# Kernel optimization log

Measured on AMD Instinct MI355X. Metric: run time of the kernel, lower is better.

The kernel has to match this reference:

```python
import jax, jax.numpy as jnp
import numpy as np

B, PD, CD = 8192, 1024, 1024


def setup_inputs() -> dict:
    key = jax.random.key(0)
    ks = jax.random.split(key, 10)
    u = lambda k, shape: jax.random.uniform(k, shape, dtype=jnp.float32, minval=-0.05, maxval=0.05)
    return {
        "P": jax.random.normal(ks[0], (B, PD), dtype=jnp.float32),
        "C1": jax.random.normal(ks[1], (B, CD), dtype=jnp.float32),
        "C2": jax.random.normal(ks[2], (B, CD), dtype=jnp.float32),
        "C3": jax.random.normal(ks[3], (B, CD), dtype=jnp.float32),
        "C4": jax.random.normal(ks[4], (B, CD), dtype=jnp.float32),
        "GateWeight_P": u(ks[5], (PD, CD)),
        "GateWeight_C": u(ks[6], (CD, CD)),
        "GateBias": u(ks[7], (CD,)),
        "OutWeight": u(ks[8], (PD, CD)),
        "OutBias": u(ks[9], (CD, 1)),
    }


def reference(P, C1, C2, C3, C4, GateWeight_P, GateWeight_C, GateBias, OutWeight, OutBias):
    # Stack the 4 choice branches: [4, B, C]
    Cs = jnp.stack([C1, C2, C3, C4], axis=0)
    WP = P @ GateWeight_P                                  # [B, C]
    WC = jnp.einsum("kbc,cd->kbd", Cs, GateWeight_C)       # [4, B, C]
    g = jax.nn.sigmoid(WP[None] + WC + GateBias)           # [4, B, C]
    C_dash = Cs * g                                        # [4, B, C]
    WP_out = P @ OutWeight                                 # [B, C]
    scores = jnp.einsum("kbc,bc->kb", C_dash, WP_out)      # batch_dot axes=[1,1]
    bias = jnp.einsum("kbc,c->kb", C_dash, OutBias[:, 0])  # K.dot(C_dash, OutBias)
    return (scores + bias).T                               # [B, 4]
```

## Files before the change

kernel.cpp:

```cpp
#include <hip/hip_runtime.h>
#include <hip/hip_bf16.h>


#define B_  8192
#define PD_ 1024
#define CD_ 1024

typedef unsigned short ushort_t;
typedef unsigned int   uint_t;
typedef __attribute__((ext_vector_type(8))) short    short8;
typedef __attribute__((ext_vector_type(4))) float    floatx4;

__device__ __forceinline__ float bf2f(unsigned short u) {
    return __uint_as_float(((unsigned)u) << 16);
}
__device__ __forceinline__ unsigned short f2bf(float f) {
    unsigned u = __float_as_uint(f);
    unsigned r = u + 0x7FFFu + ((u >> 16) & 1u);
    return (unsigned short)(r >> 16);
}

__global__ __launch_bounds__(256) void prep_kernel(const float* __restrict__ P,
                                                   const float* __restrict__ C1,
                                                   const float* __restrict__ C2,
                                                   const float* __restrict__ C3,
                                                   const float* __restrict__ C4,
                                                   const float* __restrict__ GWP,
                                                   const float* __restrict__ OW,
                                                   const float* __restrict__ GWC,
                                                   ushort_t* __restrict__ Pb,
                                                   ushort_t* __restrict__ Call,
                                                   ushort_t* __restrict__ Wcat,
                                                   ushort_t* __restrict__ GWCt,
                                                   float* __restrict__ out) {
    const int bid = blockIdx.x;
    const int tid = threadIdx.x;
    if (bid < 40960) {
        const int seg = bid >> 13;
        const int i   = (bid & 8191) * 256 + tid;
        const float* src;
        ushort_t* dst;
        switch (seg) {
            case 0: src = P;  dst = Pb; break;
            case 1: src = C1; dst = Call; break;
            case 2: src = C2; dst = Call + (size_t)1 * B_ * CD_; break;
            case 3: src = C3; dst = Call + (size_t)2 * B_ * CD_; break;
            default: src = C4; dst = Call + (size_t)3 * B_ * CD_; break;
        }
        float4 v = ((const float4*)src)[i];
        ushort4 o;
        o.x = f2bf(v.x); o.y = f2bf(v.y); o.z = f2bf(v.z); o.w = f2bf(v.w);
        ((ushort4*)dst)[i] = o;
    } else if (bid < 44032) {
        __shared__ float tile[32][33];
        const int tb  = bid - 40960;
        const int seg = tb >> 10;
        const int t32 = tb & 1023;
        const float* src;
        ushort_t* dst;
        switch (seg) {
            case 0: src = GWP; dst = Wcat; break;
            case 1: src = OW;  dst = Wcat + 1024 * 1024; break;
            default: src = GWC; dst = GWCt; break;
        }
        const int c0 = (t32 & 31) * 32, r0 = (t32 >> 5) * 32;
        const int x = tid & 31, y = tid >> 5;
        for (int i = y; i < 32; i += 8)
            tile[i][x] = src[(size_t)(r0 + i) * 1024 + c0 + x];
        __syncthreads();
        for (int i = y; i < 32; i += 8)
            dst[(size_t)(c0 + i) * 1024 + r0 + x] = f2bf(tile[x][i]);
    } else {
        const int i = (bid - 44032) * 256 + tid;
        ((float4*)out)[i] = float4{0.f, 0.f, 0.f, 0.f};
    }
}

__device__ __forceinline__ void gl_lds16(const void* g, void* l) {
    __builtin_amdgcn_global_load_lds((const __attribute__((address_space(1))) void*)g,
                                     (__attribute__((address_space(3))) void*)l, 16, 0, 0);
}

#define VM8()  asm volatile("s_waitcnt vmcnt(8)" ::: "memory")
#define VM4()  asm volatile("s_waitcnt vmcnt(4)" ::: "memory")
#define VM0()  asm volatile("s_waitcnt vmcnt(0)" ::: "memory")
#define BARR() __builtin_amdgcn_s_barrier()

__device__ __forceinline__ void gemm256_pipeline(const ushort_t* __restrict__ A,
                                                 const ushort_t* __restrict__ Bt,
                                                 int tileM, int tileN,
                                                 ushort_t* smem,
                                                 floatx4 (&acc)[8][4]) {
    const int K = 1024;
    const int t = threadIdx.x;
    const int w = t >> 6, lane = t & 63;
    const int quad = lane >> 4, l16 = lane & 15;
    const int wm = w >> 2, wn = w & 3;

    const int segg = ((lane & 3) ^ ((lane >> 3) & 3)) * 8;
    const ushort_t* Ap0 = A  + (size_t)(tileM + w * 16 + (lane >> 2)) * K + segg;
    const ushort_t* Ap1 = Ap0 + (size_t)128 * K;
    const ushort_t* Bp0 = Bt + (size_t)(tileN + w * 16 + (lane >> 2)) * K + segg;
    const ushort_t* Bp1 = Bp0 + (size_t)128 * K;
    const int lA0 = w * 512 + lane * 8;
    const int lA1 = lA0 + 4096;
    const int lB0 = 8192 + lA0;
    const int lB1 = lB0 + 4096;

    const int xs  = (quad ^ ((l16 >> 1) & 3)) * 8;
    const int roA = (wm * 128 + l16) * 32 + xs;
    const int roB = 8192 + (wn * 64 + l16) * 32 + xs;

#pragma unroll
    for (int i = 0; i < 8; i++)
#pragma unroll
        for (int j = 0; j < 4; j++) acc[i][j] = (floatx4)0.f;

#define STAGE(kt) do {                                                       \
        const int base_ = ((kt) & 3) * 16384; const int k0_ = (kt) * 32;     \
        gl_lds16(Ap0 + k0_, &smem[base_ + lA0]);                             \
        gl_lds16(Ap1 + k0_, &smem[base_ + lA1]);                             \
        gl_lds16(Bp0 + k0_, &smem[base_ + lB0]);                             \
        gl_lds16(Bp1 + k0_, &smem[base_ + lB1]); } while (0)

#define COMPUTE(kt) do {                                                     \
        const int base_ = ((kt) & 3) * 16384;                                \
        short8 af_[8], bf_[4];                                               \
        _Pragma("unroll")                                                    \
        for (int mi = 0; mi < 8; mi++)                                       \
            af_[mi] = *(const short8*)&smem[base_ + roA + mi * 512];         \
        _Pragma("unroll")                                                    \
        for (int ni = 0; ni < 4; ni++)                                       \
            bf_[ni] = *(const short8*)&smem[base_ + roB + ni * 512];         \
        __builtin_amdgcn_s_setprio(1);                                       \
        _Pragma("unroll")                                                    \
        for (int mi = 0; mi < 8; mi++)                                       \
        _Pragma("unroll")                                                    \
        for (int ni = 0; ni < 4; ni++)                                       \
            acc[mi][ni] = __builtin_amdgcn_mfma_f32_16x16x32_bf16(           \
                af_[mi], bf_[ni], acc[mi][ni], 0, 0, 0);                     \
        __builtin_amdgcn_s_setprio(0); } while (0)

    STAGE(0); STAGE(1); STAGE(2);
#pragma unroll 4
    for (int kt = 0; kt < 28; ++kt) {
        VM8(); BARR();
        STAGE(kt + 3);
        COMPUTE(kt);
    }
    VM8(); BARR(); STAGE(31); COMPUTE(28);
    VM8(); BARR(); COMPUTE(29);
    VM4(); BARR(); COMPUTE(30);
    VM0(); BARR(); COMPUTE(31);
#undef STAGE
#undef COMPUTE
}

__global__ __launch_bounds__(512, 2) void gemmA_k(const ushort_t* __restrict__ A,
                                                  const ushort_t* __restrict__ Bt,
                                                  ushort_t* __restrict__ C) {
    __shared__ ushort_t smem[65536];
    const int xcd = blockIdx.x & 7, q = blockIdx.x >> 3;
    const int tileM = ((q >> 3) * 8 + xcd) * 256;
    const int tileN = (q & 7) * 256;

    floatx4 acc[8][4];
    gemm256_pipeline(A, Bt, tileM, tileN, smem, acc);

    const int t = threadIdx.x, lane = t & 63, quad = lane >> 4, l16 = lane & 15;
    const int w = t >> 6, wm = w >> 2, wn = w & 3;
    const int rowb = tileM + wm * 128 + quad * 4;
#pragma unroll
    for (int mi = 0; mi < 8; mi++)
#pragma unroll
        for (int ni = 0; ni < 4; ni++) {
            const int col = tileN + wn * 64 + ni * 16 + l16;
            const int ci = col & 1023, hi = col >> 10;
#pragma unroll
            for (int r = 0; r < 4; r++) {
                const int row = rowb + mi * 16 + r;
                C[(size_t)(row * 1024 + ci) * 2 + hi] = f2bf(acc[mi][ni][r]);
            }
        }
}

__global__ __launch_bounds__(512, 2) void gemmB_fused(const ushort_t* __restrict__ Call,
                                                      const ushort_t* __restrict__ GWCt,
                                                      const uint_t* __restrict__ WPcat,
                                                      const float* __restrict__ Gb,
                                                      const float* __restrict__ Ob,
                                                      float* __restrict__ out) {
    __shared__ ushort_t smem[65536];
    const int xcd = blockIdx.x & 7, q = blockIdx.x >> 3;
    const int tileM = ((q >> 2) * 8 + xcd) * 256;
    const int tileN = (q & 3) * 256;

    floatx4 acc[8][4];
    gemm256_pipeline(Call, GWCt, tileM, tileN, smem, acc);

    const int t = threadIdx.x, lane = t & 63, quad = lane >> 4, l16 = lane & 15;
    const int w = t >> 6, wm = w >> 2, wn = w & 3;

    const int kk    = tileM >> 13;
    const int b0    = (tileM & 8191) + wm * 128 + quad * 4;
    const int rowg0 = tileM + wm * 128 + quad * 4;

    float gbv[4], obv[4];
    int   gcol[4];
#pragma unroll
    for (int ni = 0; ni < 4; ni++) {
        gcol[ni] = tileN + wn * 64 + ni * 16 + l16;
        gbv[ni]  = Gb[gcol[ni]];
        obv[ni]  = Ob[gcol[ni]];
    }

#pragma unroll
    for (int mi = 0; mi < 8; mi++) {
        float part[4] = {0.f, 0.f, 0.f, 0.f};
#pragma unroll
        for (int ni = 0; ni < 4; ni++) {
            const uint_t*   wpp = WPcat + (size_t)(b0 + mi * 16) * 1024 + gcol[ni];
            const ushort_t* ckp = Call  + (size_t)(rowg0 + mi * 16) * 1024 + gcol[ni];
#pragma unroll
            for (int r = 0; r < 4; r++) {
                const uint_t wpair = wpp[(size_t)r * 1024];
                const float wp  = bf2f((unsigned short)(wpair & 0xffffu));
                const float wpo = bf2f((unsigned short)(wpair >> 16));
                const float ck  = bf2f(ckp[(size_t)r * 1024]);
                const float x = wp + acc[mi][ni][r] + gbv[ni];
                const float g = 1.f / (1.f + __expf(-x));
                part[r] += ck * g * (wpo + obv[ni]);
            }
        }
#pragma unroll
        for (int r = 0; r < 4; r++) {
            part[r] += __shfl_xor(part[r], 1);
            part[r] += __shfl_xor(part[r], 2);
            part[r] += __shfl_xor(part[r], 4);
            part[r] += __shfl_xor(part[r], 8);
        }
        if (l16 == 0) {
#pragma unroll
            for (int r = 0; r < 4; r++)
                atomicAdd(&out[(size_t)(b0 + mi * 16 + r) * 4 + kk], part[r]);
        }
    }
}

extern "C" void kernel_launch(void* const* d_in, const int* in_sizes, int n_in,
                              void* d_out, int out_size, void* d_ws, size_t ws_size,
                              hipStream_t stream) {
    (void)in_sizes; (void)n_in; (void)out_size; (void)ws_size;
    const float* P   = (const float*)d_in[0];
    const float* C1  = (const float*)d_in[1];
    const float* C2  = (const float*)d_in[2];
    const float* C3  = (const float*)d_in[3];
    const float* C4  = (const float*)d_in[4];
    const float* GWP = (const float*)d_in[5];
    const float* GWC = (const float*)d_in[6];
    const float* Gb  = (const float*)d_in[7];
    const float* OW  = (const float*)d_in[8];
    const float* Ob  = (const float*)d_in[9];
    float* out = (float*)d_out;

    char* ws = (char*)d_ws;
    ushort_t* Pb    = (ushort_t*)(ws);
    ushort_t* Call  = (ushort_t*)(ws + (16u << 20));
    ushort_t* Wcat  = (ushort_t*)(ws + (80u << 20));
    ushort_t* GWCt  = (ushort_t*)(ws + (84u << 20));
    ushort_t* WPcat = (ushort_t*)(ws + (86u << 20));

    prep_kernel<<<44064, 256, 0, stream>>>(P, C1, C2, C3, C4, GWP, OW, GWC,
                                           Pb, Call, Wcat, GWCt, out);
    gemmA_k<<<256, 512, 0, stream>>>(Pb, Wcat, WPcat);
    gemmB_fused<<<512, 512, 0, stream>>>(Call, GWCt, (const uint_t*)WPcat, Gb, Ob, out);
}
```

Before: 356.9 us.

## Interleave LDS reads, global prefetch and MFMA in barrier-fenced sub-phases

Splits each K-step of the bf16 GEMM main loop into four sub-phases. Each phase loads two A fragments (and B up front), issues half of the next global-to-LDS stage, then runs MFMAs, with s_barrier and sched_barrier fences between phases. The aim is a ping-pong schedule where the waves of a block alternate memory and matrix work, and register pressure drops from holding all 8 A fragments at once. The cost is many extra barriers per K-step, and the compiler can no longer reorder instructions across the fences.

```diff
diff --git a/kernel.cpp b/kernel.cpp
--- a/kernel.cpp
+++ b/kernel.cpp
@@ -85,6 +85,7 @@
 #define VM4()  asm volatile("s_waitcnt vmcnt(4)" ::: "memory")
 #define VM0()  asm volatile("s_waitcnt vmcnt(0)" ::: "memory")
 #define BARR() __builtin_amdgcn_s_barrier()
+#define SB0()  __builtin_amdgcn_sched_barrier(0)
 
 __device__ __forceinline__ void gemm256_pipeline(const ushort_t* __restrict__ A,
                                                  const ushort_t* __restrict__ Bt,
@@ -116,44 +117,64 @@
 #pragma unroll
         for (int j = 0; j < 4; j++) acc[i][j] = (floatx4)0.f;
 
-#define STAGE(kt) do {                                                       \
-        const int base_ = ((kt) & 3) * 16384; const int k0_ = (kt) * 32;     \
-        gl_lds16(Ap0 + k0_, &smem[base_ + lA0]);                             \
-        gl_lds16(Ap1 + k0_, &smem[base_ + lA1]);                             \
-        gl_lds16(Bp0 + k0_, &smem[base_ + lB0]);                             \
-        gl_lds16(Bp1 + k0_, &smem[base_ + lB1]); } while (0)
-
-#define COMPUTE(kt) do {                                                     \
-        const int base_ = ((kt) & 3) * 16384;                                \
-        short8 af_[8], bf_[4];                                               \
-        _Pragma("unroll")                                                    \
-        for (int mi = 0; mi < 8; mi++)                                       \
-            af_[mi] = *(const short8*)&smem[base_ + roA + mi * 512];         \
-        _Pragma("unroll")                                                    \
-        for (int ni = 0; ni < 4; ni++)                                       \
-            bf_[ni] = *(const short8*)&smem[base_ + roB + ni * 512];         \
-        __builtin_amdgcn_s_setprio(1);                                       \
-        _Pragma("unroll")                                                    \
-        for (int mi = 0; mi < 8; mi++)                                       \
-        _Pragma("unroll")                                                    \
-        for (int ni = 0; ni < 4; ni++)                                       \
-            acc[mi][ni] = __builtin_amdgcn_mfma_f32_16x16x32_bf16(           \
-                af_[mi], bf_[ni], acc[mi][ni], 0, 0, 0);                     \
-        __builtin_amdgcn_s_setprio(0); } while (0)
-
-    STAGE(0); STAGE(1); STAGE(2);
-#pragma unroll 4
+#define RD8(off) (*(const short8*)&smem[(off)])
+
+#define STG_A(skt) do { const int b2_ = ((skt) & 3) * 16384; const int k2_ = (skt) * 32; \
+        gl_lds16(Ap0 + k2_, &smem[b2_ + lA0]);                                           \
+        gl_lds16(Ap1 + k2_, &smem[b2_ + lA1]); } while (0)
+#define STG_B(skt) do { const int b2_ = ((skt) & 3) * 16384; const int k2_ = (skt) * 32; \
+        gl_lds16(Bp0 + k2_, &smem[b2_ + lB0]);                                           \
+        gl_lds16(Bp1 + k2_, &smem[b2_ + lB1]); } while (0)
+#define STG4(skt) do { STG_A(skt); STG_B(skt); } while (0)
+
+#define MM(mi_, a_) do { _Pragma("unroll")                                    \
+        for (int ni = 0; ni < 4; ni++)                                        \
+            acc[mi_][ni] = __builtin_amdgcn_mfma_f32_16x16x32_bf16(           \
+                (a_), bf_[ni], acc[mi_][ni], 0, 0, 0); } while (0)
+
+#define KSTEP(kt_, skt_, DOSTG_, VMW_) do {                                   \
+        const int cb_ = ((kt_) & 3) * 16384;                                  \
+        short8 bf_[4], a0_, a1_;                                              \
+        VMW_; BARR(); SB0();                                                  \
+        _Pragma("unroll")                                                     \
+        for (int ni = 0; ni < 4; ni++) bf_[ni] = RD8(cb_ + roB + ni * 512);   \
+        a0_ = RD8(cb_ + roA + 0 * 512); a1_ = RD8(cb_ + roA + 1 * 512);       \
+        if (DOSTG_) STG_A(skt_);                                              \
+        BARR(); SB0();                                                        \
+        __builtin_amdgcn_s_setprio(1); MM(0, a0_); MM(1, a1_);                \
+        __builtin_amdgcn_s_setprio(0);                                        \
+        BARR(); SB0();                                                        \
+        a0_ = RD8(cb_ + roA + 2 * 512); a1_ = RD8(cb_ + roA + 3 * 512);       \
+        if (DOSTG_) STG_B(skt_);                                              \
+        BARR(); SB0();                                                        \
+        __builtin_amdgcn_s_setprio(1); MM(2, a0_); MM(3, a1_);                \
+        __builtin_amdgcn_s_setprio(0);                                        \
+        BARR(); SB0();                                                        \
+        a0_ = RD8(cb_ + roA + 4 * 512); a1_ = RD8(cb_ + roA + 5 * 512);       \
+        BARR(); SB0();                                                        \
+        __builtin_amdgcn_s_setprio(1); MM(4, a0_); MM(5, a1_);                \
+        __builtin_amdgcn_s_setprio(0);                                        \
+        BARR(); SB0();                                                        \
+        a0_ = RD8(cb_ + roA + 6 * 512); a1_ = RD8(cb_ + roA + 7 * 512);       \
+        BARR(); SB0();                                                        \
+        __builtin_amdgcn_s_setprio(1); MM(6, a0_); MM(7, a1_);                \
+        __builtin_amdgcn_s_setprio(0);                                        \
+    } while (0)
+
+    STG4(0); STG4(1); STG4(2);
     for (int kt = 0; kt < 28; ++kt) {
-        VM8(); BARR();
-        STAGE(kt + 3);
-        COMPUTE(kt);
-    }
-    VM8(); BARR(); STAGE(31); COMPUTE(28);
-    VM8(); BARR(); COMPUTE(29);
-    VM4(); BARR(); COMPUTE(30);
-    VM0(); BARR(); COMPUTE(31);
-#undef STAGE
-#undef COMPUTE
+        KSTEP(kt, kt + 3, 1, VM8());
+    }
+    KSTEP(28, 31, 1, VM8());
+    KSTEP(29, 0, 0, VM8());
+    KSTEP(30, 0, 0, VM4());
+    KSTEP(31, 0, 0, VM0());
+#undef KSTEP
+#undef MM
+#undef STG4
+#undef STG_B
+#undef STG_A
+#undef RD8
 }
 
 __global__ __launch_bounds__(512, 2) void gemmA_k(const ushort_t* __restrict__ A,
```

Result: no change. 360.5 us (+1.0%).
